# Kernel optimization log

Hardware: AMD Instinct MI355X
Metric: run time of the kernel (lower is better)

## Reference

```python
import jax, jax.numpy as jnp
import numpy as np

# dims
B, N, T, F, D = 16, 64, 168, 8, 248   # batch, stations, seq, features, gcn_dim
E = D + F                              # transformer dmodel = 256
H = 8                                  # attention heads
FF = 4 * E                             # expansion_factor * dmodel


def _layer_norm(x, g, b, eps=1e-5):
    m = jnp.mean(x, axis=-1, keepdims=True)
    v = jnp.var(x, axis=-1, keepdims=True)
    return (x - m) * jax.lax.rsqrt(v + eps) * g + b


def setup_inputs() -> dict:
    key = jax.random.key(0)
    ks = jax.random.split(key, 20)
    s = 0.02
    return {
        'x': jax.random.normal(ks[0], (B, N, T, F), jnp.float32),
        'locs': jax.random.uniform(ks[1], (B, N, 2), jnp.float32),
        'pos_em': jax.random.normal(ks[2], (B, T, E), jnp.float32),
        'periodic_em': jax.random.normal(ks[3], (B, T, E), jnp.float32),
        'gcn_w': jax.random.normal(ks[4], (F, D), jnp.float32) * s,
        'gcn_b': jnp.zeros((D,), jnp.float32),
        'fc1_w': jax.random.normal(ks[5], (D, D), jnp.float32) * s,
        'fc1_b': jnp.zeros((D,), jnp.float32),
        'wq': jax.random.normal(ks[6], (E, E), jnp.float32) * s,
        'bq': jnp.zeros((E,), jnp.float32),
        'wk': jax.random.normal(ks[7], (E, E), jnp.float32) * s,
        'bk': jnp.zeros((E,), jnp.float32),
        'wv': jax.random.normal(ks[8], (E, E), jnp.float32) * s,
        'bv': jnp.zeros((E,), jnp.float32),
        'wo': jax.random.normal(ks[9], (E, E), jnp.float32) * s,
        'bo': jnp.zeros((E,), jnp.float32),
        'ln1_g': jnp.ones((E,), jnp.float32),
        'ln1_b': jnp.zeros((E,), jnp.float32),
        'ln2_g': jnp.ones((E,), jnp.float32),
        'ln2_b': jnp.zeros((E,), jnp.float32),
        'ff1_w': jax.random.normal(ks[10], (E, FF), jnp.float32) * s,
        'ff1_b': jnp.zeros((FF,), jnp.float32),
        'ff2_w': jax.random.normal(ks[11], (FF, E), jnp.float32) * s,
        'ff2_b': jnp.zeros((E,), jnp.float32),
    }


def reference(x, locs, pos_em, periodic_em, gcn_w, gcn_b, fc1_w, fc1_b,
              wq, bq, wk, bk, wv, bv, wo, bo,
              ln1_g, ln1_b, ln2_g, ln2_b, ff1_w, ff1_b, ff2_w, ff2_b):
    b, n, t, f = x.shape
    # --- inverse-distance-weighted dense adjacency (fully connected graph) ---
    diff = locs[:, :, None, :] - locs[:, None, :, :]            # [B,N,N,2]
    dist = jnp.sqrt(jnp.sum(diff * diff, -1) + 1e-12)           # [B,N,N]
    w = jnp.where(jnp.eye(n, dtype=bool), 0.0, 1.0 / dist)      # no self edges
    w = w / jnp.sum(w, -1, keepdims=True)                       # norm=True
    # --- GCNConv (self loops + symmetric normalization), batched over B and T ---
    a = w + jnp.eye(n, dtype=x.dtype)
    dinv = jax.lax.rsqrt(jnp.sum(a, -1))
    a = a * dinv[:, :, None] * dinv[:, None, :]                 # [B,N,N]
    h = jnp.einsum('bntf,fd->bntd', x, gcn_w)                   # xW
    g = jax.nn.relu(jnp.einsum('bmn,bntd->bmtd', a, h) + gcn_b) # aggregate + relu
    g = jnp.einsum('bntd,de->bnte', g, fc1_w) + fc1_b           # fc1
    # --- concat features, flatten stations into batch, add positional embedding ---
    tok = jnp.concatenate([x, g], -1).reshape(b * n, t, -1)     # [B*N,T,E]
    tok = tok + jnp.repeat(pos_em, n, axis=0)                   # dropout=identity (eval)
    per = jnp.repeat(periodic_em, n, axis=0)
    # --- transformer encoder layer (periodic embedding conditions Q/K) ---
    e = tok.shape[-1]
    dh = e // H
    qk_in = tok + per
    q = (qk_in @ wq + bq).reshape(b * n, t, H, dh)
    k = (qk_in @ wk + bk).reshape(b * n, t, H, dh)
    v = (tok @ wv + bv).reshape(b * n, t, H, dh)
    s = jnp.einsum('bthd,bshd->bhts', q, k) * (1.0 / float(np.sqrt(dh)))
    p = jax.nn.softmax(s, axis=-1)
    o = jnp.einsum('bhts,bshd->bthd', p, v).reshape(b * n, t, e)
    o = o @ wo + bo
    h1 = _layer_norm(tok + o, ln1_g, ln1_b)
    ff = jax.nn.relu(h1 @ ff1_w + ff1_b) @ ff2_w + ff2_b
    out = _layer_norm(h1 + ff, ln2_g, ln2_b)
    return out.reshape(b, n, t, e)
```

## Files before the change

### kernel.cpp

```cpp
#include <hip/hip_runtime.h>
#include <hip/hip_bf16.h>

constexpr int B_  = 16;
constexpr int N_  = 64;
constexpr int T_  = 168;
constexpr int F_  = 8;
constexpr int E_  = 256;
constexpr int H_  = 8;
constexpr int DH_ = 32;
constexpr int NT_ = N_ * T_;
constexpr int LDQ_ = 768;

typedef __bf16 bf16x8 __attribute__((ext_vector_type(8)));
typedef float  f32x4  __attribute__((ext_vector_type(4)));
typedef float  f32x4u __attribute__((ext_vector_type(4), aligned(4)));

__device__ __forceinline__ unsigned short f2b(float f) {
  union { float f; unsigned int u; } v; v.f = f;
  unsigned int r = (v.u + 0x7FFFu + ((v.u >> 16) & 1u)) >> 16;
  return (unsigned short)r;
}
__device__ __forceinline__ float b2f(unsigned short h) {
  union { unsigned int u; float f; } v; v.u = ((unsigned int)h) << 16;
  return v.f;
}
__device__ __forceinline__ unsigned int cvtpk(float lo, float hi) {
  unsigned int r;
  asm("v_cvt_pk_bf16_f32 %0, %1, %2" : "=v"(r) : "v"(lo), "v"(hi));
  return r;
}
__device__ __forceinline__ void gload16(const void* g, void* l) {
  __builtin_amdgcn_global_load_lds(
      (const __attribute__((address_space(1))) unsigned int*)g,
      (__attribute__((address_space(3))) unsigned int*)l, 16, 0, 0);
}

__global__ void adj_kernel(const float* __restrict__ locs, float* __restrict__ a) {
  int b = blockIdx.x;
  int m = threadIdx.x;
  __shared__ float lx[64], ly[64];
  lx[m] = locs[(b * 64 + m) * 2 + 0];
  ly[m] = locs[(b * 64 + m) * 2 + 1];
  __syncthreads();
  float x = lx[m], y = ly[m];
  float sum = 0.f;
  for (int n = 0; n < 64; ++n) {
    float dx = x - lx[n], dy = y - ly[n];
    float d = sqrtf(dx * dx + dy * dy + 1e-12f);
    sum += (n == m) ? 0.f : 1.f / d;
  }
  float inv = 0.5f / sum;
  for (int n = 0; n < 64; ++n) {
    float dx = x - lx[n], dy = y - ly[n];
    float d = sqrtf(dx * dx + dy * dy + 1e-12f);
    float w = (n == m) ? 0.5f : inv / d;
    a[(b * 64 + m) * 64 + n] = w;
  }
}

__global__ void convw_kernel(const float* __restrict__ in, unsigned short* __restrict__ outT,
                             int K, int N, int Kp, int Np) {
  int idx = blockIdx.x * 256 + threadIdx.x;
  if (idx >= Np * Kp) return;
  int n = idx / Kp, k = idx % Kp;
  float v = (k < K && n < N) ? in[(long)k * N + n] : 0.f;
  outT[idx] = f2b(v);
}

__global__ __launch_bounds__(256) void gcn_kernel(
    const float* __restrict__ x, const float* __restrict__ adj,
    const float* __restrict__ gcn_w, const float* __restrict__ gcn_b,
    const float* __restrict__ pos_em, const float* __restrict__ per_em,
    unsigned short* __restrict__ G, unsigned short* __restrict__ tokb,
    unsigned short* __restrict__ qkb, int b0) {
  int bl = blockIdx.x / T_;
  int t = blockIdx.x % T_;
  int b = b0 + bl;
  int tid = threadIdx.x;
  __shared__ float sX[512];
  __shared__ float sXA[512];
  const float* adjb = adj + b * 4096;
  for (int i = tid; i < 512; i += 256) {
    int n = i >> 3, f = i & 7;
    sX[i] = x[((long)(b * 64 + n) * T_ + t) * F_ + f];
  }
  __syncthreads();
  for (int i = tid; i < 512; i += 256) {
    int m = i >> 3, f = i & 7;
    float s = 0.f;
    for (int n = 0; n < 64; ++n) s += adjb[(m << 6) + n] * sX[(n << 3) + f];
    sXA[i] = s;
  }
  {
    long pbase = ((long)bl * T_ + t) * E_;
    for (int i = tid; i < 512; i += 256) {
      int m = i >> 3, f = i & 7;
      long lrow = (long)(bl * 64 + m) * T_ + t;
      float base = sX[i] + pos_em[pbase + f];
      tokb[lrow * E_ + f] = f2b(base);
      qkb[lrow * E_ + f]  = f2b(base + per_em[pbase + f]);
    }
  }
  __syncthreads();
  for (int i = tid; i < 64 * 256; i += 256) {
    int m = i >> 8, d = i & 255;
    float v = 0.f;
    if (d < 248) {
      float s = gcn_b[d];
      const float* xam = &sXA[m << 3];
#pragma unroll
      for (int f = 0; f < 8; ++f) s += xam[f] * gcn_w[f * 248 + d];
      v = fmaxf(s, 0.f);
    }
    long lrow = (long)(bl * 64 + m) * T_ + t;
    G[lrow * 256 + d] = f2b(v);
  }
}

template <int KCHUNKS>
__global__ __launch_bounds__(256) void block_gemm(
    const unsigned short* __restrict__ A, int lda,
    const unsigned short* __restrict__ Bt, int K, int Nact,
    const float* __restrict__ bias,
    float* Cf, unsigned short* Cb1, unsigned short* Cb2,
    const float* __restrict__ emb1, const float* __restrict__ emb2,
    const unsigned short* __restrict__ resb, const float* resf,
    int c0, int ldc, int relu) {
  __shared__ unsigned short As[64 * 256];
  const int tid = threadIdx.x;
  const int lane = tid & 63, w = tid >> 6;
  const int l15 = lane & 15, lg = lane >> 4;
  const int m0 = blockIdx.x * 64;
  const int n0w = blockIdx.y * 256 + w * 64;

  f32x4 acc[4][4];
#pragma unroll
  for (int i = 0; i < 4; ++i)
#pragma unroll
    for (int j = 0; j < 4; ++j) acc[i][j] = (f32x4){0.f, 0.f, 0.f, 0.f};

  for (int kc = 0; kc < KCHUNKS; ++kc) {
    if (kc) __syncthreads();
#pragma unroll
    for (int j = 0; j < 8; ++j) {
      int idx = j * 256 + tid;
      int row = idx >> 5, g = idx & 31;
      int swg = (g & 24) | ((g & 7) ^ (row & 7));
      gload16(A + (long)(m0 + row) * lda + kc * 256 + swg * 8,
              &As[(j * 256 + w * 64) * 8]);
    }
    bf16x8 Wa[4], Wb[4], Xf[4];
    auto ldw = [&](bf16x8 (&W)[4], int ks) {
#pragma unroll
      for (int nf = 0; nf < 4; ++nf)
        W[nf] = *reinterpret_cast<const bf16x8*>(
            Bt + (long)(n0w + nf * 16 + l15) * K + kc * 256 + ks * 32 + (lg << 3));
    };
    auto ldx = [&](int ks) {
#pragma unroll
      for (int mf = 0; mf < 4; ++mf) {
        int row = (mf << 4) + l15;
        int ksg = (ks << 2) + lg;
        int sw = (ksg & 24) | ((ksg & 7) ^ (row & 7));
        Xf[mf] = *reinterpret_cast<const bf16x8*>(&As[((row << 5) + sw) * 8]);
      }
    };
    auto mm = [&](bf16x8 (&W)[4]) {
#pragma unroll
      for (int mf = 0; mf < 4; ++mf)
#pragma unroll
        for (int nf = 0; nf < 4; ++nf)
          acc[mf][nf] = __builtin_amdgcn_mfma_f32_16x16x32_bf16(W[nf], Xf[mf], acc[mf][nf], 0, 0, 0);
    };
    ldw(Wa, 0);
    asm volatile("s_waitcnt vmcnt(0)" ::: "memory");
    __syncthreads();
#pragma unroll
    for (int kp = 0; kp < 4; ++kp) {
      ldw(Wb, kp * 2 + 1);
      ldx(kp * 2);
      mm(Wa);
      if (kp < 3) ldw(Wa, kp * 2 + 2);
      ldx(kp * 2 + 1);
      mm(Wb);
    }
  }

  const int cb = lg << 2;
#pragma unroll
  for (int mf = 0; mf < 4; ++mf) {
    int rr = m0 + (mf << 4) + l15;
    int ar = (rr / NT_) * T_ + (rr % T_);
    long rbase  = (long)rr * ldc + c0;
    long rbase2 = (long)rr * 256 + c0;
    long abase  = (long)ar * 256 + c0;
#pragma unroll
    for (int nf = 0; nf < 4; ++nf) {
      int gcol = n0w + (nf << 4) + cb;
      if (gcol < Nact) {
        float v0 = acc[mf][nf][0], v1 = acc[mf][nf][1];
        float v2 = acc[mf][nf][2], v3 = acc[mf][nf][3];
        if (bias) {
          f32x4u b4 = *reinterpret_cast<const f32x4u*>(bias + gcol);
          v0 += b4[0]; v1 += b4[1]; v2 += b4[2]; v3 += b4[3];
        }
        if (relu) {
          v0 = fmaxf(v0, 0.f); v1 = fmaxf(v1, 0.f);
          v2 = fmaxf(v2, 0.f); v3 = fmaxf(v3, 0.f);
        }
        if (resb) {
          ushort4 rv = *reinterpret_cast<const ushort4*>(resb + rbase2 + gcol);
          v0 += b2f(rv.x); v1 += b2f(rv.y); v2 += b2f(rv.z); v3 += b2f(rv.w);
        }
        if (resf) {
          f32x4u r4 = *reinterpret_cast<const f32x4u*>(resf + rbase + gcol);
          v0 += r4[0]; v1 += r4[1]; v2 += r4[2]; v3 += r4[3];
        }
        if (emb1) {
          f32x4u e4 = *reinterpret_cast<const f32x4u*>(emb1 + abase + gcol);
          v0 += e4[0]; v1 += e4[1]; v2 += e4[2]; v3 += e4[3];
        }
        if (Cf) {
          f32x4u o; o[0] = v0; o[1] = v1; o[2] = v2; o[3] = v3;
          *reinterpret_cast<f32x4u*>(Cf + rbase + gcol) = o;
        }
        if (Cb1) {
          uint2 p = {cvtpk(v0, v1), cvtpk(v2, v3)};
          *reinterpret_cast<uint2*>(Cb1 + rbase + gcol) = p;
        }
        if (Cb2) {
          f32x4u e4 = *reinterpret_cast<const f32x4u*>(emb2 + abase + gcol);
          uint2 p = {cvtpk(v0 + e4[0], v1 + e4[1]), cvtpk(v2 + e4[2], v3 + e4[3])};
          *reinterpret_cast<uint2*>(Cb2 + rbase + gcol) = p;
        }
      }
    }
  }
}

__global__ __launch_bounds__(256) void wo_ln_kernel(
    const unsigned short* __restrict__ A, int lda,
    const unsigned short* __restrict__ Wt,
    const float* __restrict__ bias,
    const unsigned short* __restrict__ resb,
    const float* __restrict__ lng, const float* __restrict__ lnb,
    unsigned short* __restrict__ outb) {
  __shared__ unsigned short As[64 * 256];
  __shared__ float red[4][4][16][2];
  const int tid = threadIdx.x;
  const int lane = tid & 63, w = tid >> 6;
  const int l15 = lane & 15, lg = lane >> 4;
  const int m0 = blockIdx.x * 64;
  const int n0w = w * 64;

  f32x4 acc[4][4];
#pragma unroll
  for (int i = 0; i < 4; ++i)
#pragma unroll
    for (int j = 0; j < 4; ++j) acc[i][j] = (f32x4){0.f, 0.f, 0.f, 0.f};

#pragma unroll
  for (int j = 0; j < 8; ++j) {
    int idx = j * 256 + tid;
    int row = idx >> 5, g = idx & 31;
    int swg = (g & 24) | ((g & 7) ^ (row & 7));
    gload16(A + (long)(m0 + row) * lda + swg * 8, &As[(j * 256 + w * 64) * 8]);
  }
  bf16x8 Wa[4], Wb[4], Xf[4];
  auto ldw = [&](bf16x8 (&W)[4], int ks) {
#pragma unroll
    for (int nf = 0; nf < 4; ++nf)
      W[nf] = *reinterpret_cast<const bf16x8*>(
          Wt + (long)(n0w + nf * 16 + l15) * 256 + ks * 32 + (lg << 3));
  };
  auto ldx = [&](int ks) {
#pragma unroll
    for (int mf = 0; mf < 4; ++mf) {
      int row = (mf << 4) + l15;
      int ksg = (ks << 2) + lg;
      int sw = (ksg & 24) | ((ksg & 7) ^ (row & 7));
      Xf[mf] = *reinterpret_cast<const bf16x8*>(&As[((row << 5) + sw) * 8]);
    }
  };
  auto mm = [&](bf16x8 (&W)[4]) {
#pragma unroll
    for (int mf = 0; mf < 4; ++mf)
#pragma unroll
      for (int nf = 0; nf < 4; ++nf)
        acc[mf][nf] = __builtin_amdgcn_mfma_f32_16x16x32_bf16(W[nf], Xf[mf], acc[mf][nf], 0, 0, 0);
  };
  ldw(Wa, 0);
  asm volatile("s_waitcnt vmcnt(0)" ::: "memory");
  __syncthreads();
#pragma unroll
  for (int kp = 0; kp < 4; ++kp) {
    ldw(Wb, kp * 2 + 1);
    ldx(kp * 2);
    mm(Wa);
    if (kp < 3) ldw(Wa, kp * 2 + 2);
    ldx(kp * 2 + 1);
    mm(Wb);
  }

  const int cb = lg << 2;
  float s[4], s2[4];
#pragma unroll
  for (int mf = 0; mf < 4; ++mf) {
    int rr = m0 + (mf << 4) + l15;
    long rbase2 = (long)rr * 256;
    s[mf] = 0.f; s2[mf] = 0.f;
#pragma unroll
    for (int nf = 0; nf < 4; ++nf) {
      int gcol = n0w + (nf << 4) + cb;
      f32x4u b4 = *reinterpret_cast<const f32x4u*>(bias + gcol);
      ushort4 rv = *reinterpret_cast<const ushort4*>(resb + rbase2 + gcol);
      float v0 = acc[mf][nf][0] + b4[0] + b2f(rv.x);
      float v1 = acc[mf][nf][1] + b4[1] + b2f(rv.y);
      float v2 = acc[mf][nf][2] + b4[2] + b2f(rv.z);
      float v3 = acc[mf][nf][3] + b4[3] + b2f(rv.w);
      acc[mf][nf][0] = v0; acc[mf][nf][1] = v1;
      acc[mf][nf][2] = v2; acc[mf][nf][3] = v3;
      s[mf] += v0 + v1 + v2 + v3;
      s2[mf] += v0 * v0 + v1 * v1 + v2 * v2 + v3 * v3;
    }
    s[mf] += __shfl_xor(s[mf], 16, 64);
    s[mf] += __shfl_xor(s[mf], 32, 64);
    s2[mf] += __shfl_xor(s2[mf], 16, 64);
    s2[mf] += __shfl_xor(s2[mf], 32, 64);
    if (lg == 0) { red[w][mf][l15][0] = s[mf]; red[w][mf][l15][1] = s2[mf]; }
  }
  __syncthreads();
#pragma unroll
  for (int mf = 0; mf < 4; ++mf) {
    float S  = red[0][mf][l15][0] + red[1][mf][l15][0] + red[2][mf][l15][0] + red[3][mf][l15][0];
    float S2 = red[0][mf][l15][1] + red[1][mf][l15][1] + red[2][mf][l15][1] + red[3][mf][l15][1];
    float mean = S * 0.00390625f;
    float var = S2 * 0.00390625f - mean * mean;
    float rs = rsqrtf(var + 1e-5f);
    int rr = m0 + (mf << 4) + l15;
    long rbase = (long)rr * 256;
#pragma unroll
    for (int nf = 0; nf < 4; ++nf) {
      int gcol = n0w + (nf << 4) + cb;
      f32x4u g4 = *reinterpret_cast<const f32x4u*>(lng + gcol);
      f32x4u t4 = *reinterpret_cast<const f32x4u*>(lnb + gcol);
      float o0 = (acc[mf][nf][0] - mean) * rs * g4[0] + t4[0];
      float o1 = (acc[mf][nf][1] - mean) * rs * g4[1] + t4[1];
      float o2 = (acc[mf][nf][2] - mean) * rs * g4[2] + t4[2];
      float o3 = (acc[mf][nf][3] - mean) * rs * g4[3] + t4[3];
      uint2 p = {cvtpk(o0, o1), cvtpk(o2, o3)};
      *reinterpret_cast<uint2*>(outb + rbase + gcol) = p;
    }
  }
}

__global__ __launch_bounds__(256) void ff_fused_kernel(
    const unsigned short* __restrict__ h1,
    const unsigned short* __restrict__ W1,
    const unsigned short* __restrict__ W2,
    const float* __restrict__ b1, const float* __restrict__ b2,
    const float* __restrict__ lng, const float* __restrict__ lnb,
    float* __restrict__ out) {
  __shared__ unsigned short h1s[64 * 256];
  __shared__ unsigned short fis[64 * 256];
  __shared__ float red[4][4][16][2];
  const int tid = threadIdx.x;
  const int lane = tid & 63, w = tid >> 6;
  const int l15 = lane & 15, lg = lane >> 4;
  const int m0 = blockIdx.x * 64;

#pragma unroll
  for (int j = 0; j < 8; ++j) {
    int idx = j * 256 + tid;
    int row = idx >> 5, g = idx & 31;
    int swg = (g & 24) | ((g & 7) ^ (row & 7));
    gload16(h1 + (long)(m0 + row) * 256 + swg * 8, &h1s[(j * 256 + w * 64) * 8]);
  }

  f32x4 acc2[4][4];
#pragma unroll
  for (int i = 0; i < 4; ++i)
#pragma unroll
    for (int j = 0; j < 4; ++j) acc2[i][j] = (f32x4){0.f, 0.f, 0.f, 0.f};

  bf16x8 Wa[4], Wb[4], Xf[4];
  auto ldw1 = [&](bf16x8 (&W)[4], int nc, int ks) {
#pragma unroll
    for (int nf = 0; nf < 4; ++nf)
      W[nf] = *reinterpret_cast<const bf16x8*>(
          W1 + (long)(nc * 256 + w * 64 + nf * 16 + l15) * 256 + ks * 32 + (lg << 3));
  };
  auto ldw2 = [&](bf16x8 (&W)[4], int nc, int ks) {
#pragma unroll
    for (int nf = 0; nf < 4; ++nf)
      W[nf] = *reinterpret_cast<const bf16x8*>(
          W2 + (long)(w * 64 + nf * 16 + l15) * 1024 + nc * 256 + ks * 32 + (lg << 3));
  };
  auto ldx = [&](const unsigned short* S, int ks) {
#pragma unroll
    for (int mf = 0; mf < 4; ++mf) {
      int row = (mf << 4) + l15;
      int ksg = (ks << 2) + lg;
      int sw = (ksg & 24) | ((ksg & 7) ^ (row & 7));
      Xf[mf] = *reinterpret_cast<const bf16x8*>(&S[((row << 5) + sw) * 8]);
    }
  };

  const int cb = lg << 2;
  bool first = true;
  for (int nc = 0; nc < 4; ++nc) {
    f32x4 acc1[4][4];
#pragma unroll
    for (int i = 0; i < 4; ++i)
#pragma unroll
      for (int j = 0; j < 4; ++j) acc1[i][j] = (f32x4){0.f, 0.f, 0.f, 0.f};
    ldw1(Wa, nc, 0);
    if (first) {
      asm volatile("s_waitcnt vmcnt(4)" ::: "memory");
      __syncthreads();
      first = false;
    }
#pragma unroll
    for (int kp = 0; kp < 4; ++kp) {
      ldw1(Wb, nc, kp * 2 + 1);
      ldx(h1s, kp * 2);
#pragma unroll
      for (int mf = 0; mf < 4; ++mf)
#pragma unroll
        for (int nf = 0; nf < 4; ++nf)
          acc1[mf][nf] = __builtin_amdgcn_mfma_f32_16x16x32_bf16(Wa[nf], Xf[mf], acc1[mf][nf], 0, 0, 0);
      if (kp < 3) ldw1(Wa, nc, kp * 2 + 2);
      ldx(h1s, kp * 2 + 1);
#pragma unroll
      for (int mf = 0; mf < 4; ++mf)
#pragma unroll
        for (int nf = 0; nf < 4; ++nf)
          acc1[mf][nf] = __builtin_amdgcn_mfma_f32_16x16x32_bf16(Wb[nf], Xf[mf], acc1[mf][nf], 0, 0, 0);
    }
    if (nc) __syncthreads();
#pragma unroll
    for (int mf = 0; mf < 4; ++mf) {
      int row = (mf << 4) + l15;
#pragma unroll
      for (int nf = 0; nf < 4; ++nf) {
        int col = w * 64 + (nf << 4) + cb;
        f32x4u b4 = *reinterpret_cast<const f32x4u*>(b1 + nc * 256 + col);
        float v0 = fmaxf(acc1[mf][nf][0] + b4[0], 0.f);
        float v1 = fmaxf(acc1[mf][nf][1] + b4[1], 0.f);
        float v2 = fmaxf(acc1[mf][nf][2] + b4[2], 0.f);
        float v3 = fmaxf(acc1[mf][nf][3] + b4[3], 0.f);
        int g = col >> 3;
        int swg = (g & 24) | ((g & 7) ^ (row & 7));
        uint2 p = {cvtpk(v0, v1), cvtpk(v2, v3)};
        *reinterpret_cast<uint2*>(&fis[((row << 5) + swg) * 8 + (col & 7)]) = p;
      }
    }
    ldw2(Wa, nc, 0);
    __syncthreads();
#pragma unroll
    for (int kp = 0; kp < 4; ++kp) {
      ldw2(Wb, nc, kp * 2 + 1);
      ldx(fis, kp * 2);
#pragma unroll
      for (int mf = 0; mf < 4; ++mf)
#pragma unroll
        for (int nf = 0; nf < 4; ++nf)
          acc2[mf][nf] = __builtin_amdgcn_mfma_f32_16x16x32_bf16(Wa[nf], Xf[mf], acc2[mf][nf], 0, 0, 0);
      if (kp < 3) ldw2(Wa, nc, kp * 2 + 2);
      ldx(fis, kp * 2 + 1);
#pragma unroll
      for (int mf = 0; mf < 4; ++mf)
#pragma unroll
        for (int nf = 0; nf < 4; ++nf)
          acc2[mf][nf] = __builtin_amdgcn_mfma_f32_16x16x32_bf16(Wb[nf], Xf[mf], acc2[mf][nf], 0, 0, 0);
    }
  }

  float s[4], s2[4];
#pragma unroll
  for (int mf = 0; mf < 4; ++mf) {
    int row = (mf << 4) + l15;
    s[mf] = 0.f; s2[mf] = 0.f;
#pragma unroll
    for (int nf = 0; nf < 4; ++nf) {
      int gcol = w * 64 + (nf << 4) + cb;
      f32x4u b4 = *reinterpret_cast<const f32x4u*>(b2 + gcol);
      int g = gcol >> 3;
      int swg = (g & 24) | ((g & 7) ^ (row & 7));
      ushort4 rv = *reinterpret_cast<const ushort4*>(&h1s[((row << 5) + swg) * 8 + (gcol & 7)]);
      float v0 = acc2[mf][nf][0] + b4[0] + b2f(rv.x);
      float v1 = acc2[mf][nf][1] + b4[1] + b2f(rv.y);
      float v2 = acc2[mf][nf][2] + b4[2] + b2f(rv.z);
      float v3 = acc2[mf][nf][3] + b4[3] + b2f(rv.w);
      acc2[mf][nf][0] = v0; acc2[mf][nf][1] = v1;
      acc2[mf][nf][2] = v2; acc2[mf][nf][3] = v3;
      s[mf] += v0 + v1 + v2 + v3;
      s2[mf] += v0 * v0 + v1 * v1 + v2 * v2 + v3 * v3;
    }
    s[mf] += __shfl_xor(s[mf], 16, 64);
    s[mf] += __shfl_xor(s[mf], 32, 64);
    s2[mf] += __shfl_xor(s2[mf], 16, 64);
    s2[mf] += __shfl_xor(s2[mf], 32, 64);
    if (lg == 0) { red[w][mf][l15][0] = s[mf]; red[w][mf][l15][1] = s2[mf]; }
  }
  __syncthreads();
#pragma unroll
  for (int mf = 0; mf < 4; ++mf) {
    float S  = red[0][mf][l15][0] + red[1][mf][l15][0] + red[2][mf][l15][0] + red[3][mf][l15][0];
    float S2 = red[0][mf][l15][1] + red[1][mf][l15][1] + red[2][mf][l15][1] + red[3][mf][l15][1];
    float mean = S * 0.00390625f;
    float var = S2 * 0.00390625f - mean * mean;
    float rs = rsqrtf(var + 1e-5f);
    int rr = m0 + (mf << 4) + l15;
    long rbase = (long)rr * 256;
#pragma unroll
    for (int nf = 0; nf < 4; ++nf) {
      int gcol = w * 64 + (nf << 4) + cb;
      f32x4u g4 = *reinterpret_cast<const f32x4u*>(lng + gcol);
      f32x4u t4 = *reinterpret_cast<const f32x4u*>(lnb + gcol);
      f32x4u o;
      o[0] = (acc2[mf][nf][0] - mean) * rs * g4[0] + t4[0];
      o[1] = (acc2[mf][nf][1] - mean) * rs * g4[1] + t4[1];
      o[2] = (acc2[mf][nf][2] - mean) * rs * g4[2] + t4[2];
      o[3] = (acc2[mf][nf][3] - mean) * rs * g4[3] + t4[3];
      *reinterpret_cast<f32x4u*>(out + rbase + gcol) = o;
    }
  }
}

__global__ __launch_bounds__(256) void attn_mfma_kernel(unsigned short* QKV) {
  int blk = blockIdx.x;
  int bn = blk >> 3, h = blk & 7;
  int tid = threadIdx.x;
  int lane = tid & 63, w = tid >> 6;

  __shared__ unsigned short Kfr[11 * 512];
  __shared__ unsigned short VT[32][200];
  __shared__ unsigned short Pb[4][16][200];

  const long qbase = (long)bn * T_ * LDQ_ + h * DH_;
  const unsigned short* Kg = QKV + qbase + 256;
  const unsigned short* V  = QKV + qbase + 512;
  const unsigned short* Q  = QKV + qbase;
  unsigned short* O = QKV + qbase;
  int l15 = lane & 15, lg = lane >> 4;

  for (int kt = w; kt < 11; kt += 4) {
    gload16(Kg + (long)(kt * 16 + l15) * LDQ_ + (lg << 3), &Kfr[kt * 512]);
  }
  for (int i = tid; i < T_ * 4; i += 256) {
    int t = i >> 2, seg = (i & 3) << 3;
    uint4 vv = *reinterpret_cast<const uint4*>(V + (long)t * LDQ_ + seg);
    const unsigned short* vs = (const unsigned short*)&vv;
#pragma unroll
    for (int j = 0; j < 8; ++j) VT[seg + j][t] = vs[j];
  }
  for (int i = tid; i < 32 * 32; i += 256) VT[i >> 5][168 + (i & 31)] = 0;
  {
    unsigned short* pflat = &Pb[0][0][0];
    for (int i = tid; i < 64 * 24; i += 256)
      pflat[(i / 24) * 200 + 176 + (i % 24)] = 0;
  }
  __syncthreads();

  const float scale = 0.17677669529663687f;
  unsigned short* Pw = &Pb[w][0][0];

  for (int it = 0; it < 3; ++it) {
    int qt = w + it * 4;
    if (qt > 10) break;
    bf16x8 af = *reinterpret_cast<const bf16x8*>(
        Q + (long)(qt * 16 + l15) * LDQ_ + (lg << 3));
    f32x4 s[11];
#pragma unroll
    for (int kt = 0; kt < 11; ++kt) {
      bf16x8 bf = *reinterpret_cast<const bf16x8*>(&Kfr[kt * 512 + lane * 8]);
      s[kt] = __builtin_amdgcn_mfma_f32_16x16x32_bf16(
          af, bf, (f32x4){0.f, 0.f, 0.f, 0.f}, 0, 0, 0);
    }
    bool ok10 = (l15 < 8);
    float inv_l[4];
#pragma unroll
    for (int r = 0; r < 4; ++r) {
      float mx = -1e30f;
#pragma unroll
      for (int kt = 0; kt < 10; ++kt) mx = fmaxf(mx, s[kt][r] * scale);
      if (ok10) mx = fmaxf(mx, s[10][r] * scale);
#pragma unroll
      for (int off = 1; off < 16; off <<= 1) mx = fmaxf(mx, __shfl_xor(mx, off, 64));
      float pv[11];
      float ls = 0.f;
#pragma unroll
      for (int kt = 0; kt < 11; ++kt) {
        bool valid = (kt < 10) || ok10;
        float p = valid ? __expf(s[kt][r] * scale - mx) : 0.f;
        pv[kt] = p;
        ls += p;
      }
#pragma unroll
      for (int off = 1; off < 16; off <<= 1) ls += __shfl_xor(ls, off, 64);
      inv_l[r] = 1.f / ls;
      int prow = (lg << 2) + r;
#pragma unroll
      for (int kt = 0; kt < 11; ++kt)
        Pw[prow * 200 + kt * 16 + l15] = f2b(pv[kt]);
    }
    asm volatile("s_waitcnt lgkmcnt(0)" ::: "memory");
    __builtin_amdgcn_sched_barrier(0);
    f32x4 o0 = (f32x4){0.f, 0.f, 0.f, 0.f};
    f32x4 o1 = (f32x4){0.f, 0.f, 0.f, 0.f};
#pragma unroll
    for (int ks = 0; ks < 6; ++ks) {
      bf16x8 pf = *reinterpret_cast<const bf16x8*>(&Pw[l15 * 200 + ks * 32 + (lg << 3)]);
      bf16x8 v0 = *reinterpret_cast<const bf16x8*>(&VT[l15][ks * 32 + (lg << 3)]);
      bf16x8 v1 = *reinterpret_cast<const bf16x8*>(&VT[16 + l15][ks * 32 + (lg << 3)]);
      o0 = __builtin_amdgcn_mfma_f32_16x16x32_bf16(pf, v0, o0, 0, 0, 0);
      o1 = __builtin_amdgcn_mfma_f32_16x16x32_bf16(pf, v1, o1, 0, 0, 0);
    }
    int rg = lg << 2;
#pragma unroll
    for (int r = 0; r < 4; ++r) {
      int q = qt * 16 + rg + r;
      if (q < T_) {
        long ob = (long)q * LDQ_;
        O[ob + l15]      = f2b(o0[r] * inv_l[r]);
        O[ob + 16 + l15] = f2b(o1[r] * inv_l[r]);
      }
    }
  }
}

extern "C" void kernel_launch(void* const* d_in, const int* in_sizes, int n_in,
                              void* d_out, int out_size, void* d_ws, size_t ws_size,
                              hipStream_t stream) {
  const float* x      = (const float*)d_in[0];
  const float* locs   = (const float*)d_in[1];
  const float* pos_em = (const float*)d_in[2];
  const float* per_em = (const float*)d_in[3];
  const float* gcn_w  = (const float*)d_in[4];
  const float* gcn_b  = (const float*)d_in[5];
  const float* fc1_w  = (const float*)d_in[6];
  const float* fc1_b  = (const float*)d_in[7];
  const float* wq = (const float*)d_in[8];
  const float* bq = (const float*)d_in[9];
  const float* wk = (const float*)d_in[10];
  const float* bk = (const float*)d_in[11];
  const float* wv = (const float*)d_in[12];
  const float* bv = (const float*)d_in[13];
  const float* wo = (const float*)d_in[14];
  const float* bo = (const float*)d_in[15];
  const float* ln1_g = (const float*)d_in[16];
  const float* ln1_b = (const float*)d_in[17];
  const float* ln2_g = (const float*)d_in[18];
  const float* ln2_b = (const float*)d_in[19];
  const float* ff1_w = (const float*)d_in[20];
  const float* ff1_b = (const float*)d_in[21];
  const float* ff2_w = (const float*)d_in[22];
  const float* ff2_b = (const float*)d_in[23];
  float* out = (float*)d_out;

  const size_t ADJ_BYTES = 1u << 20;
  const size_t WB_BYTES  = 2u << 20;
  int CB = 16;
  while (CB > 1) {
    if (ADJ_BYTES + WB_BYTES + (size_t)CB * NT_ * 2560 <= ws_size) break;
    CB >>= 1;
  }
  char* ws = (char*)d_ws;
  float* adj = (float*)ws;
  unsigned short* wslab = (unsigned short*)(ws + ADJ_BYTES);
  unsigned short* fc1T  = wslab;
  unsigned short* wqkT  = wslab + 65536;
  unsigned short* wkT   = wslab + 2 * 65536;
  unsigned short* wvT   = wslab + 3 * 65536;
  unsigned short* woT   = wslab + 4 * 65536;
  unsigned short* ff1T  = wslab + 5 * 65536;
  unsigned short* ff2T  = wslab + 5 * 65536 + 262144;
  float* bqk = (float*)(ws + ADJ_BYTES + 1900544);

  unsigned short* tokb = (unsigned short*)(ws + ADJ_BYTES + WB_BYTES);
  unsigned short* qkb  = tokb + (size_t)CB * NT_ * 256;
  unsigned short* qkv  = qkb + (size_t)CB * NT_ * 256;
  unsigned short* h1b  = tokb;

  adj_kernel<<<B_, 64, 0, stream>>>(locs, adj);
  convw_kernel<<<256, 256, 0, stream>>>(fc1_w, fc1T, 248, 248, 256, 256);
  convw_kernel<<<256, 256, 0, stream>>>(wq, wqkT, 256, 256, 256, 256);
  convw_kernel<<<256, 256, 0, stream>>>(wk, wkT, 256, 256, 256, 256);
  convw_kernel<<<256, 256, 0, stream>>>(wv, wvT, 256, 256, 256, 256);
  convw_kernel<<<256, 256, 0, stream>>>(wo, woT, 256, 256, 256, 256);
  convw_kernel<<<1024, 256, 0, stream>>>(ff1_w, ff1T, 256, 1024, 256, 1024);
  convw_kernel<<<1024, 256, 0, stream>>>(ff2_w, ff2T, 1024, 256, 1024, 256);
  hipMemcpyAsync(bqk, bq, 256 * sizeof(float), hipMemcpyDeviceToDevice, stream);
  hipMemcpyAsync(bqk + 256, bk, 256 * sizeof(float), hipMemcpyDeviceToDevice, stream);

  for (int b0 = 0; b0 < B_; b0 += CB) {
    const int rows = CB * NT_;
    const int GX = rows / 64;
    const float* pos_c = pos_em + (long)b0 * T_ * E_;
    const float* per_c = per_em + (long)b0 * T_ * E_;
    float* out_c = out + (long)b0 * NT_ * E_;
    unsigned short* G = qkv;

    gcn_kernel<<<CB * T_, 256, 0, stream>>>(x, adj, gcn_w, gcn_b, pos_c, per_c,
                                            G, tokb, qkb, b0);
    block_gemm<1><<<dim3(GX, 1), 256, 0, stream>>>(
        G, 256, fc1T, 256, 248, fc1_b, nullptr, tokb, qkb, pos_c, per_c,
        nullptr, nullptr, 8, 256, 0);
    block_gemm<1><<<dim3(GX, 2), 256, 0, stream>>>(
        qkb, 256, wqkT, 256, 512, bqk, nullptr, qkv, nullptr, nullptr, nullptr,
        nullptr, nullptr, 0, LDQ_, 0);
    block_gemm<1><<<dim3(GX, 1), 256, 0, stream>>>(
        tokb, 256, wvT, 256, 256, bv, nullptr, qkv, nullptr, nullptr, nullptr,
        nullptr, nullptr, 512, LDQ_, 0);
    attn_mfma_kernel<<<CB * N_ * H_, 256, 0, stream>>>(qkv);
    wo_ln_kernel<<<GX, 256, 0, stream>>>(qkv, LDQ_, woT, bo, tokb,
                                         ln1_g, ln1_b, h1b);
    ff_fused_kernel<<<GX, 256, 0, stream>>>(h1b, ff1T, ff2T, ff1_b, ff2_b,
                                            ln2_g, ln2_b, out_c);
  }
}
```

Before: 1.196 ms.

## Shrink FF hidden chunk to 128 and use 8-wave block for QK GEMM

The fused FF kernel now processes the 1024-wide hidden dimension in eight chunks of 128 instead of four of 256. This halves the intermediate LDS buffer and the first-GEMM accumulator registers, aiming for higher occupancy at the cost of more barriers per block. The block GEMM gains a wave-count template parameter, and the Q/K projection now runs as one 512-thread block per row tile instead of two 256-thread blocks. That lets one block load the shared A tile once for both Q and K outputs.

```diff
diff --git a/kernel.cpp b/kernel.cpp
--- a/kernel.cpp
+++ b/kernel.cpp
@@ -117,8 +117,8 @@
   }
 }
 
-template <int KCHUNKS>
-__global__ __launch_bounds__(256) void block_gemm(
+template <int KCHUNKS, int WAVES>
+__global__ __launch_bounds__(WAVES * 64) void block_gemm(
     const unsigned short* __restrict__ A, int lda,
     const unsigned short* __restrict__ Bt, int K, int Nact,
     const float* __restrict__ bias,
@@ -131,7 +131,7 @@
   const int lane = tid & 63, w = tid >> 6;
   const int l15 = lane & 15, lg = lane >> 4;
   const int m0 = blockIdx.x * 64;
-  const int n0w = blockIdx.y * 256 + w * 64;
+  const int n0w = blockIdx.y * (WAVES * 64) + w * 64;
 
   f32x4 acc[4][4];
 #pragma unroll
@@ -142,12 +142,12 @@
   for (int kc = 0; kc < KCHUNKS; ++kc) {
     if (kc) __syncthreads();
 #pragma unroll
-    for (int j = 0; j < 8; ++j) {
-      int idx = j * 256 + tid;
+    for (int j = 0; j < 32 / WAVES; ++j) {
+      int idx = j * (WAVES * 64) + tid;
       int row = idx >> 5, g = idx & 31;
       int swg = (g & 24) | ((g & 7) ^ (row & 7));
       gload16(A + (long)(m0 + row) * lda + kc * 256 + swg * 8,
-              &As[(j * 256 + w * 64) * 8]);
+              &As[(j * (WAVES * 64) + w * 64) * 8]);
     }
     bf16x8 Wa[4], Wb[4], Xf[4];
     auto ldw = [&](bf16x8 (&W)[4], int ks) {
@@ -362,7 +362,7 @@
     const float* __restrict__ lng, const float* __restrict__ lnb,
     float* __restrict__ out) {
   __shared__ unsigned short h1s[64 * 256];
-  __shared__ unsigned short fis[64 * 256];
+  __shared__ unsigned short fis[64 * 128];
   __shared__ float red[4][4][16][2];
   const int tid = threadIdx.x;
   const int lane = tid & 63, w = tid >> 6;
@@ -383,91 +383,100 @@
 #pragma unroll
     for (int j = 0; j < 4; ++j) acc2[i][j] = (f32x4){0.f, 0.f, 0.f, 0.f};
 
-  bf16x8 Wa[4], Wb[4], Xf[4];
-  auto ldw1 = [&](bf16x8 (&W)[4], int nc, int ks) {
+  bf16x8 W1a[2], W1b[2], Wa[4], Wb[4], Xf[4];
+  auto ldw1 = [&](bf16x8 (&W)[2], int hc, int ks) {
+#pragma unroll
+    for (int nf = 0; nf < 2; ++nf)
+      W[nf] = *reinterpret_cast<const bf16x8*>(
+          W1 + (long)(hc * 128 + w * 32 + nf * 16 + l15) * 256 + ks * 32 + (lg << 3));
+  };
+  auto ldw2 = [&](bf16x8 (&W)[4], int hc, int ks) {
 #pragma unroll
     for (int nf = 0; nf < 4; ++nf)
       W[nf] = *reinterpret_cast<const bf16x8*>(
-          W1 + (long)(nc * 256 + w * 64 + nf * 16 + l15) * 256 + ks * 32 + (lg << 3));
+          W2 + (long)(w * 64 + nf * 16 + l15) * 1024 + hc * 128 + ks * 32 + (lg << 3));
   };
-  auto ldw2 = [&](bf16x8 (&W)[4], int nc, int ks) {
-#pragma unroll
-    for (int nf = 0; nf < 4; ++nf)
-      W[nf] = *reinterpret_cast<const bf16x8*>(
-          W2 + (long)(w * 64 + nf * 16 + l15) * 1024 + nc * 256 + ks * 32 + (lg << 3));
-  };
-  auto ldx = [&](const unsigned short* S, int ks) {
+  auto ldxh = [&](int ks) {
 #pragma unroll
     for (int mf = 0; mf < 4; ++mf) {
       int row = (mf << 4) + l15;
       int ksg = (ks << 2) + lg;
       int sw = (ksg & 24) | ((ksg & 7) ^ (row & 7));
-      Xf[mf] = *reinterpret_cast<const bf16x8*>(&S[((row << 5) + sw) * 8]);
+      Xf[mf] = *reinterpret_cast<const bf16x8*>(&h1s[((row << 5) + sw) * 8]);
+    }
+  };
+  auto ldxf = [&](int ks) {
+#pragma unroll
+    for (int mf = 0; mf < 4; ++mf) {
+      int row = (mf << 4) + l15;
+      int ksg = (ks << 2) + lg;
+      int sw = (ksg & 8) | ((ksg & 7) ^ (row & 7));
+      Xf[mf] = *reinterpret_cast<const bf16x8*>(&fis[((row << 4) + sw) * 8]);
     }
   };
 
   const int cb = lg << 2;
   bool first = true;
-  for (int nc = 0; nc < 4; ++nc) {
-    f32x4 acc1[4][4];
+  for (int hc = 0; hc < 8; ++hc) {
+    f32x4 acc1[4][2];
 #pragma unroll
     for (int i = 0; i < 4; ++i)
 #pragma unroll
-      for (int j = 0; j < 4; ++j) acc1[i][j] = (f32x4){0.f, 0.f, 0.f, 0.f};
-    ldw1(Wa, nc, 0);
+      for (int j = 0; j < 2; ++j) acc1[i][j] = (f32x4){0.f, 0.f, 0.f, 0.f};
+    ldw1(W1a, hc, 0);
     if (first) {
-      asm volatile("s_waitcnt vmcnt(4)" ::: "memory");
+      asm volatile("s_waitcnt vmcnt(2)" ::: "memory");
       __syncthreads();
       first = false;
     }
 #pragma unroll
     for (int kp = 0; kp < 4; ++kp) {
-      ldw1(Wb, nc, kp * 2 + 1);
-      ldx(h1s, kp * 2);
+      ldw1(W1b, hc, kp * 2 + 1);
+      ldxh(kp * 2);
 #pragma unroll
       for (int mf = 0; mf < 4; ++mf)
 #pragma unroll
-        for (int nf = 0; nf < 4; ++nf)
-          acc1[mf][nf] = __builtin_amdgcn_mfma_f32_16x16x32_bf16(Wa[nf], Xf[mf], acc1[mf][nf], 0, 0, 0);
-      if (kp < 3) ldw1(Wa, nc, kp * 2 + 2);
-      ldx(h1s, kp * 2 + 1);
+        for (int nf = 0; nf < 2; ++nf)
+          acc1[mf][nf] = __builtin_amdgcn_mfma_f32_16x16x32_bf16(W1a[nf], Xf[mf], acc1[mf][nf], 0, 0, 0);
+      if (kp < 3) ldw1(W1a, hc, kp * 2 + 2);
+      ldxh(kp * 2 + 1);
 #pragma unroll
       for (int mf = 0; mf < 4; ++mf)
 #pragma unroll
-        for (int nf = 0; nf < 4; ++nf)
-          acc1[mf][nf] = __builtin_amdgcn_mfma_f32_16x16x32_bf16(Wb[nf], Xf[mf], acc1[mf][nf], 0, 0, 0);
-    }
-    if (nc) __syncthreads();
+        for (int nf = 0; nf < 2; ++nf)
+          acc1[mf][nf] = __builtin_amdgcn_mfma_f32_16x16x32_bf16(W1b[nf], Xf[mf], acc1[mf][nf], 0, 0, 0);
+    }
+    if (hc) __syncthreads();
 #pragma unroll
     for (int mf = 0; mf < 4; ++mf) {
       int row = (mf << 4) + l15;
 #pragma unroll
-      for (int nf = 0; nf < 4; ++nf) {
-        int col = w * 64 + (nf << 4) + cb;
-        f32x4u b4 = *reinterpret_cast<const f32x4u*>(b1 + nc * 256 + col);
+      for (int nf = 0; nf < 2; ++nf) {
+        int col = w * 32 + (nf << 4) + cb;
+        f32x4u b4 = *reinterpret_cast<const f32x4u*>(b1 + hc * 128 + col);
         float v0 = fmaxf(acc1[mf][nf][0] + b4[0], 0.f);
         float v1 = fmaxf(acc1[mf][nf][1] + b4[1], 0.f);
         float v2 = fmaxf(acc1[mf][nf][2] + b4[2], 0.f);
         float v3 = fmaxf(acc1[mf][nf][3] + b4[3], 0.f);
         int g = col >> 3;
-        int swg = (g & 24) | ((g & 7) ^ (row & 7));
+        int swg = (g & 8) | ((g & 7) ^ (row & 7));
         uint2 p = {cvtpk(v0, v1), cvtpk(v2, v3)};
-        *reinterpret_cast<uint2*>(&fis[((row << 5) + swg) * 8 + (col & 7)]) = p;
+        *reinterpret_cast<uint2*>(&fis[((row << 4) + swg) * 8 + (col & 7)]) = p;
       }
     }
-    ldw2(Wa, nc, 0);
+    ldw2(Wa, hc, 0);
     __syncthreads();
 #pragma unroll
-    for (int kp = 0; kp < 4; ++kp) {
-      ldw2(Wb, nc, kp * 2 + 1);
-      ldx(fis, kp * 2);
+    for (int kp = 0; kp < 2; ++kp) {
+      ldw2(Wb, hc, kp * 2 + 1);
+      ldxf(kp * 2);
 #pragma unroll
       for (int mf = 0; mf < 4; ++mf)
 #pragma unroll
         for (int nf = 0; nf < 4; ++nf)
           acc2[mf][nf] = __builtin_amdgcn_mfma_f32_16x16x32_bf16(Wa[nf], Xf[mf], acc2[mf][nf], 0, 0, 0);
-      if (kp < 3) ldw2(Wa, nc, kp * 2 + 2);
-      ldx(fis, kp * 2 + 1);
+      if (kp < 1) ldw2(Wa, hc, kp * 2 + 2);
+      ldxf(kp * 2 + 1);
 #pragma unroll
       for (int mf = 0; mf < 4; ++mf)
 #pragma unroll
@@ -704,13 +713,13 @@
 
     gcn_kernel<<<CB * T_, 256, 0, stream>>>(x, adj, gcn_w, gcn_b, pos_c, per_c,
                                             G, tokb, qkb, b0);
-    block_gemm<1><<<dim3(GX, 1), 256, 0, stream>>>(
+    block_gemm<1, 4><<<dim3(GX, 1), 256, 0, stream>>>(
         G, 256, fc1T, 256, 248, fc1_b, nullptr, tokb, qkb, pos_c, per_c,
         nullptr, nullptr, 8, 256, 0);
-    block_gemm<1><<<dim3(GX, 2), 256, 0, stream>>>(
+    block_gemm<1, 8><<<dim3(GX, 1), 512, 0, stream>>>(
         qkb, 256, wqkT, 256, 512, bqk, nullptr, qkv, nullptr, nullptr, nullptr,
         nullptr, nullptr, 0, LDQ_, 0);
-    block_gemm<1><<<dim3(GX, 1), 256, 0, stream>>>(
+    block_gemm<1, 4><<<dim3(GX, 1), 256, 0, stream>>>(
         tokb, 256, wvT, 256, 256, bv, nullptr, qkv, nullptr, nullptr, nullptr,
         nullptr, nullptr, 512, LDQ_, 0);
     attn_mfma_kernel<<<CB * N_ * H_, 256, 0, stream>>>(qkv);
```

Measured after the change: 1.153 ms. -3.6%, faster.
